# Kernel optimization log

Measured on AMD Instinct MI355X. Metric: run time of the kernel, lower is better.

Reference implementation:

```python
import jax, jax.numpy as jnp
import numpy as np

N_NODES = 100000
N_EDGES = 3200000
D = 32


def _gat(x, edge_index, W, att_s, att_d, bias, heads, ch, neg_slope):
    """PyG-style GATConv (shared lin for src/dst, add_self_loops=False).
    x: [N, D_in], edge_index: [2, E], W: [heads*ch, D_in],
    att_s/att_d: [heads, ch], bias: [heads*ch]. Returns [N, heads*ch]."""
    n = x.shape[0]
    h = (x @ W.T).reshape(n, heads, ch)                      # [N,H,C]
    a_s = (h * att_s[None]).sum(-1)                           # [N,H]
    a_d = (h * att_d[None]).sum(-1)                           # [N,H]
    src, dst = edge_index[0], edge_index[1]
    logits = jax.nn.leaky_relu(a_s[src] + a_d[dst], neg_slope)  # [E,H]
    # segment softmax over edges grouped by destination node
    m = jax.ops.segment_max(logits, dst, num_segments=n)     # [N,H]
    m = jnp.where(jnp.isfinite(m), m, 0.0)                    # nodes w/ no in-edges
    ex = jnp.exp(logits - m[dst])                             # [E,H]
    denom = jax.ops.segment_sum(ex, dst, num_segments=n)     # [N,H]
    alpha = ex / (denom[dst] + 1e-16)                         # [E,H]
    out = jax.ops.segment_sum(alpha[:, :, None] * h[src], dst, num_segments=n)  # [N,H,C]
    return out.reshape(n, heads * ch) + bias


def setup_inputs() -> dict:
    key = jax.random.key(0)
    ks = jax.random.split(key, 16)
    x = jax.random.normal(ks[0], (N_NODES, D), dtype=jnp.float32)
    edge_index = jax.random.randint(ks[1], (2, N_EDGES), 0, N_NODES, dtype=jnp.int64)
    s = 1.0 / np.sqrt(D)
    return {
        "x": x,
        "edge_index": edge_index,
        "W1": jax.random.normal(ks[2], (32, D), dtype=jnp.float32) * s,
        "att_s1": jax.random.normal(ks[3], (2, 16), dtype=jnp.float32) * 0.05,
        "att_d1": jax.random.normal(ks[4], (2, 16), dtype=jnp.float32) * 0.05,
        "b1": jnp.full((32,), 0.1, dtype=jnp.float32),
        "ea1": jnp.ones((1,), dtype=jnp.float32),  # edge_activator
        "W2": jax.random.normal(ks[5], (32, 32), dtype=jnp.float32) * s,
        "att_s2": jax.random.normal(ks[6], (2, 16), dtype=jnp.float32) * 0.05,
        "att_d2": jax.random.normal(ks[7], (2, 16), dtype=jnp.float32) * 0.05,
        "b2": jnp.full((32,), 0.1, dtype=jnp.float32),
        "W3": jax.random.normal(ks[8], (32, 32), dtype=jnp.float32) * s,
        "att_s3": jax.random.normal(ks[9], (1, 32), dtype=jnp.float32) * 0.05,
        "att_d3": jax.random.normal(ks[10], (1, 32), dtype=jnp.float32) * 0.05,
        "b3": jnp.full((32,), 0.1, dtype=jnp.float32),
    }


def reference(x, edge_index, W1, att_s1, att_d1, b1, ea1,
              W2, att_s2, att_d2, b2, W3, att_s3, att_d3, b3):
    # --- layer 1 (negative_slope=0.01) ---
    h = _gat(x, edge_index, W1, att_s1, att_d1, b1, heads=2, ch=16, neg_slope=0.01)
    scale = jnp.tanh(ea1)[0]
    scale = jnp.where(scale < 0.1, 1.0, scale)  # 'continue' branch skips the scaling
    h = h * scale
    h = h + 0.05 * jax.lax.stop_gradient(h)      # h + 0.05*h.detach()
    h = jax.nn.elu(h)                            # eval path (training=False)
    h = jnp.clip(h, -3.0, 3.0)
    # --- layer 2 (default negative_slope=0.2) ---
    h = _gat(h, edge_index, W2, att_s2, att_d2, b2, heads=2, ch=16, neg_slope=0.2)
    h = jax.nn.elu(h)
    h = jnp.clip(h, -3.0, 3.0)
    # --- layer 3: heads=1, concat=False ---
    out = _gat(h, edge_index, W3, att_s3, att_d3, b3, heads=1, ch=32, neg_slope=0.2)
    return out
```

## Files before the change

kernel.cpp:

```cpp
#include <hip/hip_runtime.h>
#include <hip/hip_bf16.h>
#include <hip/hip_fp16.h>


#define NPB  128
#define CAPB 6144
#define PAD_SENTINEL 0xFFFFFFFFu

__global__ void __launch_bounds__(1024)
k_bin(const int* __restrict__ src, const int* __restrict__ dst,
      int* __restrict__ bucket_cursor, unsigned int* __restrict__ pairs,
      int e, int nb) {
    __shared__ int h[1024];
    __shared__ int bs[1024];
    __shared__ int cb[1024];
    __shared__ unsigned int stage[8192];
    int t = threadIdx.x;
    h[t] = 0;
    __syncthreads();
    int e4 = e >> 2;
    int base4 = blockIdx.x * 2048;
    int boff[8];
    unsigned int pk[8];
#pragma unroll
    for (int k = 0; k < 2; k++) {
        int i4 = base4 + k * 1024 + t;
        if (i4 < e4) {
            int4 dv = ((const int4*)dst)[i4];
            int4 sv = ((const int4*)src)[i4];
            const int* dd = (const int*)&dv;
            const int* ss = (const int*)&sv;
#pragma unroll
            for (int j = 0; j < 4; j++) {
                int q = 4 * k + j;
                int d = dd[j];
                int b = d >> 7;
                pk[q] = ((unsigned int)ss[j] << 7) | (unsigned int)(d & 127);
                int off = atomicAdd(&h[b], 1);
                boff[q] = (b << 16) | off;
            }
        } else {
#pragma unroll
            for (int j = 0; j < 4; j++) boff[4 * k + j] = -1;
        }
    }
    __syncthreads();
    if (t >= 128 && t - 128 < nb) {
        int b = t - 128;
        int c = h[b];
        cb[b] = c ? atomicAdd(&bucket_cursor[b], c) : 0;
    }
    if (t < 64) {
        int sum = 0;
#pragma unroll
        for (int j = 0; j < 16; j++) sum += h[t * 16 + j];
        int run = sum;
#pragma unroll
        for (int off = 1; off < 64; off <<= 1) {
            int v = __shfl_up(run, off, 64);
            if (t >= off) run += v;
        }
        int base = run - sum;
#pragma unroll
        for (int j = 0; j < 16; j++) {
            int b = t * 16 + j;
            bs[b] = base;
            base += h[b];
        }
    }
    __syncthreads();
#pragma unroll
    for (int q = 0; q < 8; q++) {
        if (boff[q] >= 0) {
            int b = boff[q] >> 16;
            stage[bs[b] + (boff[q] & 0xFFFF)] = pk[q];
        }
    }
    __syncthreads();
    int wv = t >> 6, ln = t & 63;
    for (int b = wv; b < nb; b += 16) {
        int c = h[b];
        if (c == 0) continue;
        int gb = cb[b];
        int room = CAPB - gb;
        if (c > room) c = (room > 0) ? room : 0;
        unsigned int* dp = pairs + (size_t)b * CAPB + gb;
        const unsigned int* sp = stage + bs[b];
        for (int o = ln; o < c; o += 64) dp[o] = sp[o];
    }
    if (blockIdx.x == 0 && t < (e & 3)) {
        int i = (e & ~3) + t;
        int d = dst[i];
        int b = d >> 7;
        int r = atomicAdd(&bucket_cursor[b], 1);
        if (r < CAPB)
            pairs[(size_t)b * CAPB + r] =
                ((unsigned int)src[i] << 7) | (unsigned int)(d & 127);
    }
}

__global__ void __launch_bounds__(512)
k_bucket_sort(const unsigned int* __restrict__ pairs,
              const int* __restrict__ bucket_cursor,
              int2* __restrict__ rowinfo, int* __restrict__ src_sorted,
              int n) {
    __shared__ int cnt[NPB];
    __shared__ int cur[NPB];
    __shared__ int total;
    __shared__ unsigned int lp[CAPB];
    __shared__ int op[CAPB];
    int b = blockIdx.x;
    int t = threadIdx.x;
    int bbase = b * CAPB;
    int m = bucket_cursor[b];
    if (m > CAPB) m = CAPB;
    if (t < NPB) cnt[t] = 0;
    __syncthreads();
    for (int cb = 0; cb < m; cb += 4096) {
        unsigned int pv[8];
#pragma unroll
        for (int u = 0; u < 8; u++) {
            int i = cb + u * 512 + t;
            pv[u] = (i < m) ? pairs[bbase + i] : PAD_SENTINEL;
        }
#pragma unroll
        for (int u = 0; u < 8; u++) {
            int i = cb + u * 512 + t;
            if (i < m) lp[i] = pv[u];
            if (pv[u] != PAD_SENTINEL) atomicAdd(&cnt[pv[u] & 127], 1);
        }
    }
    __syncthreads();
    if (t < 64) {
        int c0 = cnt[2 * t];
        int c1 = cnt[2 * t + 1];
        int sum = c0 + c1;
        int run = sum;
#pragma unroll
        for (int off = 1; off < 64; off <<= 1) {
            int v = __shfl_up(run, off, 64);
            if (t >= off) run += v;
        }
        int ex = run - sum;
        cur[2 * t] = ex;
        cur[2 * t + 1] = ex + c0;
        int node = b * NPB + 2 * t;
        if (node < n) rowinfo[node] = make_int2(bbase + ex, c0);
        if (node + 1 < n) rowinfo[node + 1] = make_int2(bbase + ex + c0, c1);
        if (t == 63) total = run;
    }
    __syncthreads();
    for (int cb = 0; cb < m; cb += 4096) {
        unsigned int pv[8];
        int of[8];
#pragma unroll
        for (int u = 0; u < 8; u++) {
            int i = cb + u * 512 + t;
            pv[u] = (i < m) ? lp[i] : PAD_SENTINEL;
        }
#pragma unroll
        for (int u = 0; u < 8; u++)
            if (pv[u] != PAD_SENTINEL) of[u] = atomicAdd(&cur[pv[u] & 127], 1);
#pragma unroll
        for (int u = 0; u < 8; u++)
            if (pv[u] != PAD_SENTINEL) op[of[u]] = (int)(pv[u] >> 7);
    }
    __syncthreads();
    int nt4 = (total + 3) >> 2;
    int4* dst4 = (int4*)(src_sorted + bbase);
    const int4* src4 = (const int4*)op;
    for (int i = t; i < nt4; i += 512) dst4[i] = src4[i];
}

template <int H>
__global__ void k_transform(const float* __restrict__ in, const float* __restrict__ W,
                            const float* __restrict__ att_s, const float* __restrict__ att_d,
                            __half* __restrict__ h16, float* __restrict__ a_s,
                            float* __restrict__ a_d, int n) {
    constexpr int C = 32 / H;
    __shared__ float Wl[32][33];
    __shared__ float xs[8][32];
    int t = threadIdx.x;
    for (int i = t; i < 1024; i += 256) Wl[i >> 5][i & 31] = W[i];
    int nl = t >> 5, o = t & 31;
    int node = blockIdx.x * 8 + nl;
    xs[nl][o] = (node < n) ? in[node * 32 + o] : 0.f;
    __syncthreads();
    float acc = 0.f;
#pragma unroll
    for (int k = 0; k < 32; k++) acc = fmaf(xs[nl][k], Wl[o][k], acc);
    if (node < n) {
        h16[node * 32 + o] = __float2half_rn(acc);
        float vs = acc * att_s[o];
        float vd = acc * att_d[o];
#pragma unroll
        for (int m = C / 2; m >= 1; m >>= 1) {
            vs += __shfl_xor(vs, m, 64);
            vd += __shfl_xor(vd, m, 64);
        }
        if ((o % C) == 0) {
            int hh = o / C;
            a_s[node * H + hh] = vs;
            a_d[node * H + hh] = vd;
        }
    }
}

template <int H, int EPI>
__global__ void k_edge(const int2* __restrict__ rowinfo, const int* __restrict__ src_sorted,
                       const __half* __restrict__ h16,
                       const float* __restrict__ a_s, const float* __restrict__ a_d,
                       const float* __restrict__ bias, const float* __restrict__ ea,
                       float* __restrict__ out, int n, float slope) {
    constexpr int CAP = 128;
    constexpr int RSTR = 2 * CAP + 16;
    __shared__ int lds_raw[8][H][RSTR];
    int nw = threadIdx.x >> 5;
    int hl = threadIdx.x & 31;
    int node = blockIdx.x * 8 + nw;
    if (node >= n) return;
    int2 bi = rowinfo[node];
    int beg = bi.x, deg = bi.y;
    int padB = (deg + 15) & ~15;

    float ad[H];
#pragma unroll
    for (int hh = 0; hh < H; hh++) ad[hh] = a_d[node * H + hh];

    float ds[H];
#pragma unroll
    for (int hh = 0; hh < H; hh++) ds[hh] = 0.f;
    bool fast = (padB <= CAP);
    if (fast) {
        for (int idx = hl; idx < padB; idx += 32) {
            if (idx < deg) {
                int s = src_sorted[beg + idx];
                if (H == 2) {
                    float2 as2 = *(const float2*)((const char*)a_s + (unsigned)(s << 3));
                    float l0 = as2.x + ad[0]; l0 = fmaxf(l0, l0 * slope);
                    float l1 = as2.y + ad[1]; l1 = fmaxf(l1, l1 * slope);
                    float e0 = __expf(l0), e1 = __expf(l1);
                    ds[0] += e0; ds[1] += e1;
                    ((int2*)lds_raw[nw][0])[idx] = make_int2(s, __float_as_int(e0));
                    ((int2*)lds_raw[nw][H - 1])[idx] = make_int2(s, __float_as_int(e1));
                } else {
                    float l0 = a_s[s] + ad[0]; l0 = fmaxf(l0, l0 * slope);
                    float e0 = __expf(l0);
                    ds[0] += e0;
                    ((int2*)lds_raw[nw][0])[idx] = make_int2(s, __float_as_int(e0));
                }
            } else {
#pragma unroll
                for (int hh = 0; hh < H; hh++)
                    ((int2*)lds_raw[nw][hh])[idx] = make_int2(0, 0);
            }
        }
    } else {
        for (int idx = hl; idx < deg; idx += 32) {
            int s = src_sorted[beg + idx];
            if (H == 2) {
                float2 as2 = *(const float2*)((const char*)a_s + (unsigned)(s << 3));
                float l0 = as2.x + ad[0]; l0 = fmaxf(l0, l0 * slope);
                float l1 = as2.y + ad[1]; l1 = fmaxf(l1, l1 * slope);
                ds[0] += __expf(l0); ds[1] += __expf(l1);
            } else {
                float l0 = a_s[s] + ad[0]; l0 = fmaxf(l0, l0 * slope);
                ds[0] += __expf(l0);
            }
        }
    }

    int e2 = hl >> 4;
    int l16 = hl & 15;
    int hd = (H == 2) ? (l16 >> 3) : 0;
    int co = l16 << 2;
    float adh = ad[hd];
    float acc0 = 0.f, acc1 = 0.f;
    const char* hbase = (const char*)h16;
    const int* lb = &lds_raw[nw][hd][e2 * 4];

    if (fast) {
        for (int base = 0; base < padB; base += 16) {
            int4 qa = *(const int4*)(lb + base * 2);
            int4 qb = *(const int4*)(lb + base * 2 + 8);
            int4 qc = *(const int4*)(lb + base * 2 + 16);
            int4 qd = *(const int4*)(lb + base * 2 + 24);
            __half2 h0 = *(const __half2*)(hbase + (unsigned)((qa.x << 6) + co));
            __half2 h1 = *(const __half2*)(hbase + (unsigned)((qa.z << 6) + co));
            __half2 h2 = *(const __half2*)(hbase + (unsigned)((qb.x << 6) + co));
            __half2 h3 = *(const __half2*)(hbase + (unsigned)((qb.z << 6) + co));
            __half2 h4 = *(const __half2*)(hbase + (unsigned)((qc.x << 6) + co));
            __half2 h5 = *(const __half2*)(hbase + (unsigned)((qc.z << 6) + co));
            __half2 h6 = *(const __half2*)(hbase + (unsigned)((qd.x << 6) + co));
            __half2 h7 = *(const __half2*)(hbase + (unsigned)((qd.z << 6) + co));
            float xa0 = __int_as_float(qa.y), xa1 = __int_as_float(qa.w);
            float xb0 = __int_as_float(qb.y), xb1 = __int_as_float(qb.w);
            float xc0 = __int_as_float(qc.y), xc1 = __int_as_float(qc.w);
            float xd0 = __int_as_float(qd.y), xd1 = __int_as_float(qd.w);
            acc0 = fmaf(xa0, __half2float(__low2half(h0)), acc0);
            acc1 = fmaf(xa0, __half2float(__high2half(h0)), acc1);
            acc0 = fmaf(xa1, __half2float(__low2half(h1)), acc0);
            acc1 = fmaf(xa1, __half2float(__high2half(h1)), acc1);
            acc0 = fmaf(xb0, __half2float(__low2half(h2)), acc0);
            acc1 = fmaf(xb0, __half2float(__high2half(h2)), acc1);
            acc0 = fmaf(xb1, __half2float(__low2half(h3)), acc0);
            acc1 = fmaf(xb1, __half2float(__high2half(h3)), acc1);
            acc0 = fmaf(xc0, __half2float(__low2half(h4)), acc0);
            acc1 = fmaf(xc0, __half2float(__high2half(h4)), acc1);
            acc0 = fmaf(xc1, __half2float(__low2half(h5)), acc0);
            acc1 = fmaf(xc1, __half2float(__high2half(h5)), acc1);
            acc0 = fmaf(xd0, __half2float(__low2half(h6)), acc0);
            acc1 = fmaf(xd0, __half2float(__high2half(h6)), acc1);
            acc0 = fmaf(xd1, __half2float(__low2half(h7)), acc0);
            acc1 = fmaf(xd1, __half2float(__high2half(h7)), acc1);
        }
    } else {
        for (int base = 0; base < deg; base += 16) {
#pragma unroll
            for (int u = 0; u < 8; u++) {
                int idx = base + u * 2 + e2;
                int s = 0;
                float ex = 0.f;
                if (idx < deg) {
                    s = src_sorted[beg + idx];
                    float l = a_s[s * H + hd] + adh;
                    l = fmaxf(l, l * slope);
                    ex = __expf(l);
                }
                __half2 hv = *(const __half2*)(hbase + (unsigned)((s << 6) + co));
                acc0 = fmaf(ex, __half2float(__low2half(hv)), acc0);
                acc1 = fmaf(ex, __half2float(__high2half(hv)), acc1);
            }
        }
    }

#pragma unroll
    for (int hh = 0; hh < H; hh++) {
        float v = ds[hh];
#pragma unroll
        for (int m = 16; m >= 1; m >>= 1) v += __shfl_xor(v, m, 64);
        ds[hh] = 1.f / (v + 1e-16f);
    }

    acc0 += __shfl_xor(acc0, 16, 64);
    acc1 += __shfl_xor(acc1, 16, 64);

    if (l16 == hl) {
        float invd = ds[hd];
        float2 bv = *(const float2*)(bias + l16 * 2);
        float v0 = fmaf(acc0, invd, bv.x);
        float v1 = fmaf(acc1, invd, bv.y);
        if (EPI == 1) {
            float s0 = tanhf(ea[0]);
            if (s0 < 0.1f) s0 = 1.0f;
            s0 *= 1.05f;
            v0 *= s0; v1 *= s0;
            v0 = (v0 > 0.f) ? v0 : expm1f(v0);
            v1 = (v1 > 0.f) ? v1 : expm1f(v1);
            v0 = fminf(3.f, fmaxf(-3.f, v0));
            v1 = fminf(3.f, fmaxf(-3.f, v1));
        } else if (EPI == 2) {
            v0 = (v0 > 0.f) ? v0 : expm1f(v0);
            v1 = (v1 > 0.f) ? v1 : expm1f(v1);
            v0 = fminf(3.f, fmaxf(-3.f, v0));
            v1 = fminf(3.f, fmaxf(-3.f, v1));
        }
        *(float2*)(out + (size_t)node * 32 + l16 * 2) = make_float2(v0, v1);
    }
}

extern "C" void kernel_launch(void* const* d_in, const int* in_sizes, int n_in,
                              void* d_out, int out_size, void* d_ws, size_t ws_size,
                              hipStream_t stream) {
    const float* x   = (const float*)d_in[0];
    const int*   ei  = (const int*)d_in[1];
    const float* W1  = (const float*)d_in[2];
    const float* as1 = (const float*)d_in[3];
    const float* ad1 = (const float*)d_in[4];
    const float* b1  = (const float*)d_in[5];
    const float* ea1 = (const float*)d_in[6];
    const float* W2  = (const float*)d_in[7];
    const float* as2 = (const float*)d_in[8];
    const float* ad2 = (const float*)d_in[9];
    const float* b2  = (const float*)d_in[10];
    const float* W3  = (const float*)d_in[11];
    const float* as3 = (const float*)d_in[12];
    const float* ad3 = (const float*)d_in[13];
    const float* b3  = (const float*)d_in[14];
    float* out = (float*)d_out;

    const int n = in_sizes[0] / 32;
    const int e = in_sizes[1] / 2;
    const int* src = ei;
    const int* dst = ei + e;
    const int nb = (n + NPB - 1) / NPB;

    char* w = (char*)d_ws;
    auto alloc = [&](size_t bytes) -> void* {
        void* p = (void*)w;
        w += (bytes + 255) & ~(size_t)255;
        return p;
    };
    __half* h16     = (__half*)alloc((size_t)n * 32 * 2);
    float* a_s      = (float*)alloc((size_t)n * 2 * 4);
    float* a_d      = (float*)alloc((size_t)n * 2 * 4);
    float* bufA     = (float*)alloc((size_t)n * 32 * 4);
    float* bufB     = (float*)alloc((size_t)n * 32 * 4);
    int2* rowinfo   = (int2*)alloc((size_t)n * 8);
    int* bucket_cur = (int*)alloc((size_t)(nb + 1) * 4);
    int* src_sorted = (int*)alloc((size_t)nb * CAPB * 4);
    unsigned int* pairs = (unsigned int*)bufA;

    hipMemsetAsync(bucket_cur, 0, (size_t)nb * 4, stream);
    int e4 = e >> 2;
    k_bin<<<(e4 + 2047) / 2048, 1024, 0, stream>>>(src, dst, bucket_cur, pairs, e, nb);
    k_bucket_sort<<<nb, 512, 0, stream>>>(pairs, bucket_cur, rowinfo, src_sorted, n);

    const int tgrid = (n + 7) / 8;
    const int egrid = (n + 7) / 8;

    k_transform<2><<<tgrid, 256, 0, stream>>>(x, W1, as1, ad1, h16, a_s, a_d, n);
    k_edge<2, 1><<<egrid, 256, 0, stream>>>(rowinfo, src_sorted, h16, a_s, a_d, b1, ea1, bufA, n, 0.01f);

    k_transform<2><<<tgrid, 256, 0, stream>>>(bufA, W2, as2, ad2, h16, a_s, a_d, n);
    k_edge<2, 2><<<egrid, 256, 0, stream>>>(rowinfo, src_sorted, h16, a_s, a_d, b2, nullptr, bufB, n, 0.2f);

    k_transform<1><<<tgrid, 256, 0, stream>>>(bufB, W3, as3, ad3, h16, a_s, a_d, n);
    k_edge<1, 0><<<egrid, 256, 0, stream>>>(rowinfo, src_sorted, h16, a_s, a_d, b3, nullptr, out, n, 0.2f);
}
```

Measured before the change: 341.8 us.

## Fuse layer-1 transform into bin and bucket-sort kernels as extra blocks

Removes the separate first-layer transform launch. Its work is split across two kernels: half the nodes are handled by extra blocks appended to the binning kernel, and the rest by extra blocks appended to the bucket-sort kernel. Shared memory is unioned so both roles fit in one kernel. This saves a launch and lets the independent transform overlap with the sort's memory-bound phases, but it adds extra blocks to those grids and may change their occupancy.

```diff
diff --git a/kernel.cpp b/kernel.cpp
--- a/kernel.cpp
+++ b/kernel.cpp
@@ -7,16 +7,60 @@
 #define CAPB 6144
 #define PAD_SENTINEL 0xFFFFFFFFu
 
+template <int H, int NL>
+__device__ __forceinline__ void transform_body(
+    const float* __restrict__ in, const float* __restrict__ W,
+    const float* __restrict__ att_s, const float* __restrict__ att_d,
+    __half* __restrict__ h16, float* __restrict__ a_s, float* __restrict__ a_d,
+    int node0, int nlim, float (*Wl)[33], float (*xs)[32]) {
+    constexpr int C = 32 / H;
+    constexpr int NTH = NL * 32;
+    int t = threadIdx.x;
+    for (int i = t; i < 1024; i += NTH) Wl[i >> 5][i & 31] = W[i];
+    int nl = t >> 5, o = t & 31;
+    int node = node0 + nl;
+    xs[nl][o] = (node < nlim) ? in[(size_t)node * 32 + o] : 0.f;
+    __syncthreads();
+    float acc = 0.f;
+#pragma unroll
+    for (int k = 0; k < 32; k++) acc = fmaf(xs[nl][k], Wl[o][k], acc);
+    if (node < nlim) {
+        h16[(size_t)node * 32 + o] = __float2half_rn(acc);
+        float vs = acc * att_s[o];
+        float vd = acc * att_d[o];
+#pragma unroll
+        for (int m = C / 2; m >= 1; m >>= 1) {
+            vs += __shfl_xor(vs, m, 64);
+            vd += __shfl_xor(vd, m, 64);
+        }
+        if ((o % C) == 0) {
+            int hh = o / C;
+            a_s[node * H + hh] = vs;
+            a_d[node * H + hh] = vd;
+        }
+    }
+}
+
 __global__ void __launch_bounds__(1024)
-k_bin(const int* __restrict__ src, const int* __restrict__ dst,
-      int* __restrict__ bucket_cursor, unsigned int* __restrict__ pairs,
-      int e, int nb) {
-    __shared__ int h[1024];
-    __shared__ int bs[1024];
-    __shared__ int cb[1024];
-    __shared__ unsigned int stage[8192];
+k_bin_t1(const int* __restrict__ src, const int* __restrict__ dst,
+         int* __restrict__ bucket_cursor, unsigned int* __restrict__ pairs,
+         int e, int nb, int nbb,
+         const float* __restrict__ in, const float* __restrict__ W,
+         const float* __restrict__ att_s, const float* __restrict__ att_d,
+         __half* __restrict__ h16, float* __restrict__ a_s,
+         float* __restrict__ a_d, int nsplit) {
+    __shared__ union {
+        struct { int h[1024]; int bs[1024]; int cb[1024]; unsigned int stage[8192]; } b;
+        struct { float Wl[32][33]; float xs[32][32]; } t;
+    } sh;
     int t = threadIdx.x;
-    h[t] = 0;
+    if ((int)blockIdx.x >= nbb) {
+        int node0 = ((int)blockIdx.x - nbb) * 32;
+        transform_body<2, 32>(in, W, att_s, att_d, h16, a_s, a_d,
+                              node0, nsplit, sh.t.Wl, sh.t.xs);
+        return;
+    }
+    sh.b.h[t] = 0;
     __syncthreads();
     int e4 = e >> 2;
     int base4 = blockIdx.x * 2048;
@@ -36,7 +80,7 @@
                 int d = dd[j];
                 int b = d >> 7;
                 pk[q] = ((unsigned int)ss[j] << 7) | (unsigned int)(d & 127);
-                int off = atomicAdd(&h[b], 1);
+                int off = atomicAdd(&sh.b.h[b], 1);
                 boff[q] = (b << 16) | off;
             }
         } else {
@@ -47,13 +91,13 @@
     __syncthreads();
     if (t >= 128 && t - 128 < nb) {
         int b = t - 128;
-        int c = h[b];
-        cb[b] = c ? atomicAdd(&bucket_cursor[b], c) : 0;
+        int c = sh.b.h[b];
+        sh.b.cb[b] = c ? atomicAdd(&bucket_cursor[b], c) : 0;
     }
     if (t < 64) {
         int sum = 0;
 #pragma unroll
-        for (int j = 0; j < 16; j++) sum += h[t * 16 + j];
+        for (int j = 0; j < 16; j++) sum += sh.b.h[t * 16 + j];
         int run = sum;
 #pragma unroll
         for (int off = 1; off < 64; off <<= 1) {
@@ -64,8 +108,8 @@
 #pragma unroll
         for (int j = 0; j < 16; j++) {
             int b = t * 16 + j;
-            bs[b] = base;
-            base += h[b];
+            sh.b.bs[b] = base;
+            base += sh.b.h[b];
         }
     }
     __syncthreads();
@@ -73,19 +117,19 @@
     for (int q = 0; q < 8; q++) {
         if (boff[q] >= 0) {
             int b = boff[q] >> 16;
-            stage[bs[b] + (boff[q] & 0xFFFF)] = pk[q];
+            sh.b.stage[sh.b.bs[b] + (boff[q] & 0xFFFF)] = pk[q];
         }
     }
     __syncthreads();
     int wv = t >> 6, ln = t & 63;
     for (int b = wv; b < nb; b += 16) {
-        int c = h[b];
+        int c = sh.b.h[b];
         if (c == 0) continue;
-        int gb = cb[b];
+        int gb = sh.b.cb[b];
         int room = CAPB - gb;
         if (c > room) c = (room > 0) ? room : 0;
         unsigned int* dp = pairs + (size_t)b * CAPB + gb;
-        const unsigned int* sp = stage + bs[b];
+        const unsigned int* sp = sh.b.stage + sh.b.bs[b];
         for (int o = ln; o < c; o += 64) dp[o] = sp[o];
     }
     if (blockIdx.x == 0 && t < (e & 3)) {
@@ -100,21 +144,31 @@
 }
 
 __global__ void __launch_bounds__(512)
-k_bucket_sort(const unsigned int* __restrict__ pairs,
-              const int* __restrict__ bucket_cursor,
-              int2* __restrict__ rowinfo, int* __restrict__ src_sorted,
-              int n) {
-    __shared__ int cnt[NPB];
-    __shared__ int cur[NPB];
-    __shared__ int total;
-    __shared__ unsigned int lp[CAPB];
-    __shared__ int op[CAPB];
+k_sort_t1(const unsigned int* __restrict__ pairs,
+          const int* __restrict__ bucket_cursor,
+          int2* __restrict__ rowinfo, int* __restrict__ src_sorted,
+          int n, int nb,
+          const float* __restrict__ in, const float* __restrict__ W,
+          const float* __restrict__ att_s, const float* __restrict__ att_d,
+          __half* __restrict__ h16, float* __restrict__ a_s,
+          float* __restrict__ a_d, int nsplit) {
+    __shared__ union {
+        struct { int cnt[NPB]; int cur[NPB]; int total;
+                 unsigned int lp[CAPB]; int op[CAPB]; } s;
+        struct { float Wl[32][33]; float xs[16][32]; } t;
+    } sh;
+    int t = threadIdx.x;
+    if ((int)blockIdx.x >= nb) {
+        int node0 = nsplit + ((int)blockIdx.x - nb) * 16;
+        transform_body<2, 16>(in, W, att_s, att_d, h16, a_s, a_d,
+                              node0, n, sh.t.Wl, sh.t.xs);
+        return;
+    }
     int b = blockIdx.x;
-    int t = threadIdx.x;
     int bbase = b * CAPB;
     int m = bucket_cursor[b];
     if (m > CAPB) m = CAPB;
-    if (t < NPB) cnt[t] = 0;
+    if (t < NPB) sh.s.cnt[t] = 0;
     __syncthreads();
     for (int cb = 0; cb < m; cb += 4096) {
         unsigned int pv[8];
@@ -126,14 +180,14 @@
 #pragma unroll
         for (int u = 0; u < 8; u++) {
             int i = cb + u * 512 + t;
-            if (i < m) lp[i] = pv[u];
-            if (pv[u] != PAD_SENTINEL) atomicAdd(&cnt[pv[u] & 127], 1);
+            if (i < m) sh.s.lp[i] = pv[u];
+            if (pv[u] != PAD_SENTINEL) atomicAdd(&sh.s.cnt[pv[u] & 127], 1);
         }
     }
     __syncthreads();
     if (t < 64) {
-        int c0 = cnt[2 * t];
-        int c1 = cnt[2 * t + 1];
+        int c0 = sh.s.cnt[2 * t];
+        int c1 = sh.s.cnt[2 * t + 1];
         int sum = c0 + c1;
         int run = sum;
 #pragma unroll
@@ -142,12 +196,12 @@
             if (t >= off) run += v;
         }
         int ex = run - sum;
-        cur[2 * t] = ex;
-        cur[2 * t + 1] = ex + c0;
+        sh.s.cur[2 * t] = ex;
+        sh.s.cur[2 * t + 1] = ex + c0;
         int node = b * NPB + 2 * t;
         if (node < n) rowinfo[node] = make_int2(bbase + ex, c0);
         if (node + 1 < n) rowinfo[node + 1] = make_int2(bbase + ex + c0, c1);
-        if (t == 63) total = run;
+        if (t == 63) sh.s.total = run;
     }
     __syncthreads();
     for (int cb = 0; cb < m; cb += 4096) {
@@ -156,19 +210,19 @@
 #pragma unroll
         for (int u = 0; u < 8; u++) {
             int i = cb + u * 512 + t;
-            pv[u] = (i < m) ? lp[i] : PAD_SENTINEL;
+            pv[u] = (i < m) ? sh.s.lp[i] : PAD_SENTINEL;
         }
 #pragma unroll
         for (int u = 0; u < 8; u++)
-            if (pv[u] != PAD_SENTINEL) of[u] = atomicAdd(&cur[pv[u] & 127], 1);
+            if (pv[u] != PAD_SENTINEL) of[u] = atomicAdd(&sh.s.cur[pv[u] & 127], 1);
 #pragma unroll
         for (int u = 0; u < 8; u++)
-            if (pv[u] != PAD_SENTINEL) op[of[u]] = (int)(pv[u] >> 7);
-    }
-    __syncthreads();
-    int nt4 = (total + 3) >> 2;
+            if (pv[u] != PAD_SENTINEL) sh.s.op[of[u]] = (int)(pv[u] >> 7);
+    }
+    __syncthreads();
+    int nt4 = (sh.s.total + 3) >> 2;
     int4* dst4 = (int4*)(src_sorted + bbase);
-    const int4* src4 = (const int4*)op;
+    const int4* src4 = (const int4*)sh.s.op;
     for (int i = t; i < nt4; i += 512) dst4[i] = src4[i];
 }
 
@@ -177,33 +231,10 @@
                             const float* __restrict__ att_s, const float* __restrict__ att_d,
                             __half* __restrict__ h16, float* __restrict__ a_s,
                             float* __restrict__ a_d, int n) {
-    constexpr int C = 32 / H;
     __shared__ float Wl[32][33];
     __shared__ float xs[8][32];
-    int t = threadIdx.x;
-    for (int i = t; i < 1024; i += 256) Wl[i >> 5][i & 31] = W[i];
-    int nl = t >> 5, o = t & 31;
-    int node = blockIdx.x * 8 + nl;
-    xs[nl][o] = (node < n) ? in[node * 32 + o] : 0.f;
-    __syncthreads();
-    float acc = 0.f;
-#pragma unroll
-    for (int k = 0; k < 32; k++) acc = fmaf(xs[nl][k], Wl[o][k], acc);
-    if (node < n) {
-        h16[node * 32 + o] = __float2half_rn(acc);
-        float vs = acc * att_s[o];
-        float vd = acc * att_d[o];
-#pragma unroll
-        for (int m = C / 2; m >= 1; m >>= 1) {
-            vs += __shfl_xor(vs, m, 64);
-            vd += __shfl_xor(vd, m, 64);
-        }
-        if ((o % C) == 0) {
-            int hh = o / C;
-            a_s[node * H + hh] = vs;
-            a_d[node * H + hh] = vd;
-        }
-    }
+    transform_body<H, 8>(in, W, att_s, att_d, h16, a_s, a_d,
+                         blockIdx.x * 8, n, Wl, xs);
 }
 
 template <int H, int EPI>
@@ -411,15 +442,23 @@
     int* src_sorted = (int*)alloc((size_t)nb * CAPB * 4);
     unsigned int* pairs = (unsigned int*)bufA;
 
+    int nsplit = n / 2;
+    nsplit = (nsplit + 31) & ~31;
+    if (nsplit > n) nsplit = n;
+    const int t1a = (nsplit + 31) / 32;
+    const int t1b = (n - nsplit + 15) / 16;
+    int e4 = e >> 2;
+    const int nbb = (e4 + 2047) / 2048;
+
     hipMemsetAsync(bucket_cur, 0, (size_t)nb * 4, stream);
-    int e4 = e >> 2;
-    k_bin<<<(e4 + 2047) / 2048, 1024, 0, stream>>>(src, dst, bucket_cur, pairs, e, nb);
-    k_bucket_sort<<<nb, 512, 0, stream>>>(pairs, bucket_cur, rowinfo, src_sorted, n);
+    k_bin_t1<<<nbb + t1a, 1024, 0, stream>>>(src, dst, bucket_cur, pairs, e, nb, nbb,
+                                             x, W1, as1, ad1, h16, a_s, a_d, nsplit);
+    k_sort_t1<<<nb + t1b, 512, 0, stream>>>(pairs, bucket_cur, rowinfo, src_sorted, n, nb,
+                                            x, W1, as1, ad1, h16, a_s, a_d, nsplit);
 
     const int tgrid = (n + 7) / 8;
     const int egrid = (n + 7) / 8;
 
-    k_transform<2><<<tgrid, 256, 0, stream>>>(x, W1, as1, ad1, h16, a_s, a_d, n);
     k_edge<2, 1><<<egrid, 256, 0, stream>>>(rowinfo, src_sorted, h16, a_s, a_d, b1, ea1, bufA, n, 0.01f);
 
     k_transform<2><<<tgrid, 256, 0, stream>>>(bufA, W2, as2, ad2, h16, a_s, a_d, n);
```

Result: no change. 335.6 us (-1.8%).
